# Kernel tuning notes

Hardware: AMD Instinct MI355X
Metric: run time of the kernel (lower is better)

Reference implementation:

```python
import jax, jax.numpy as jnp
import numpy as np

THR_CONF = 0.5   # threshold_conf
THR_NMS = 0.3    # threshold_nms
K = 1024         # fixed pre-NMS top-k per image (jit-friendly stand-in for boolean filter)
VAR0, VAR1 = 0.1, 0.2  # SSD/RetinaFace decode variances


def setup_inputs() -> dict:
    key = jax.random.key(0)
    k1, k2, k3, k4 = jax.random.split(key, 4)
    B, N = 64, 16800
    p_loc = jax.random.normal(k1, (B, N, 4), jnp.float32)
    p_conf = jax.random.normal(k2, (B, N, 1), jnp.float32)
    p_landms = jax.random.normal(k3, (B, N, 10), jnp.float32)
    # anchor priors in cxcywh, normalized coords
    anchors = jax.random.uniform(k4, (N, 4), jnp.float32, 0.05, 0.6)
    return {"p_loc": p_loc, "p_conf": p_conf, "p_landms": p_landms, "anchors": anchors}


def _decode_boxes(anchors, loc):
    # fix_bbox: cxcy = a_cxcy + loc_xy * var0 * a_wh ; wh = a_wh * exp(loc_wh * var1)
    xy = anchors[..., :2] + loc[..., :2] * VAR0 * anchors[..., 2:]
    wh = anchors[..., 2:] * jnp.exp(loc[..., 2:] * VAR1)
    # xywh2ltrb
    return jnp.concatenate([xy - wh * 0.5, xy + wh * 0.5], axis=-1)  # (B,N,4)


def _decode_kpts(anchors, landms):
    # fix_keypoints: 5 points, each = a_cxcy + d * var0 * a_wh
    B, N, _ = landms.shape
    pts = landms.reshape(B, N, 5, 2)
    kp = anchors[:, None, :2] + pts * VAR0 * anchors[:, None, 2:]
    return kp.reshape(B, N, 10)


def _iou_matrix(b):  # b: (K,4) ltrb -> (K,K)
    area = jnp.maximum(b[:, 2] - b[:, 0], 0.0) * jnp.maximum(b[:, 3] - b[:, 1], 0.0)
    lt = jnp.maximum(b[:, None, :2], b[None, :, :2])
    rb = jnp.minimum(b[:, None, 2:], b[None, :, 2:])
    wh = jnp.maximum(rb - lt, 0.0)
    inter = wh[..., 0] * wh[..., 1]
    return inter / (area[:, None] + area[None, :] - inter + 1e-9)


def _nms_one(boxes, kpts, scores):
    # boxes (N,4), kpts (N,10), scores (N,)
    s = jnp.where(scores >= THR_CONF, scores, -1.0)  # conf mask
    vals, idx = jax.lax.top_k(s, K)                  # sorted candidates (torch nms sorts by score)
    b = boxes[idx]
    kp = kpts[idx]
    iou = _iou_matrix(b)
    ar = jnp.arange(K)

    def body(suppressed, i):
        keep_i = (vals[i] >= THR_CONF) & (~suppressed[i])
        suppressed = suppressed | (keep_i & (iou[i] > THR_NMS) & (ar > i))
        return suppressed, keep_i

    _, keep = jax.lax.scan(body, jnp.zeros(K, dtype=bool), ar)
    m = keep.astype(b.dtype)[:, None]
    # (K,15) = ltrb(4) | keypoints(10) | score(1), zeroed where suppressed/filtered
    return jnp.concatenate([b, kp, vals[:, None]], axis=-1) * m


def reference(p_loc, p_conf, p_landms, anchors):
    scores = jax.nn.sigmoid(p_conf)[..., 0]       # (B,N)
    boxes = _decode_boxes(anchors, p_loc)         # (B,N,4) ltrb
    kpts = _decode_kpts(anchors, p_landms)        # (B,N,10)
    return jax.vmap(_nms_one)(boxes, kpts, scores)  # (B,K,15)
```

## Files before the change

kernel.cpp:

```cpp
#include <hip/hip_runtime.h>
#include <cmath>

#define NB 64
#define NN 16800
#define KK 1024
#define NT 1024
#define CAP 2048
#define RQ 17

typedef unsigned long long ull;

__device__ __forceinline__ unsigned int score_key_f(float cf) {
  if (!(cf >= 0.0f)) return 0u;
  return (__float_as_uint(cf) & 0x7FFFFFFFu) + 1u;
}

__device__ __forceinline__ unsigned int bin_of_key(unsigned int key) {
  float cf = __uint_as_float(key - 1u);
  unsigned int bi = (unsigned int)(int)(cf * 1024.0f);
  return bi > 4095u ? 4095u : bi;
}

__device__ __forceinline__ ull score_key_d(float cf) {
  double s = 1.0 / (1.0 + exp(-(double)cf));
  if (!(s >= 0.5)) return 0ull;
  return ((ull)__double_as_longlong(s) & 0xFFFFFFFFFFFFFull) + 1ull;
}

__device__ __forceinline__ void decode_box_d(const float* lp, const float* ap,
                                             double& X0, double& Y0,
                                             double& X1, double& Y1,
                                             double& AR) {
#pragma clang fp contract(off)
  double l0 = (double)lp[0], l1 = (double)lp[1];
  double l2 = (double)lp[2], l3 = (double)lp[3];
  double a0 = (double)ap[0], a1 = (double)ap[1];
  double a2 = (double)ap[2], a3 = (double)ap[3];
  double xy0 = a0 + (l0 * 0.1) * a2;
  double xy1 = a1 + (l1 * 0.1) * a3;
  double w = a2 * exp(l2 * 0.2);
  double h = a3 * exp(l3 * 0.2);
  X0 = xy0 - w * 0.5; Y0 = xy1 - h * 0.5;
  X1 = xy0 + w * 0.5; Y1 = xy1 + h * 0.5;
  AR = fmax(X1 - X0, 0.0) * fmax(Y1 - Y0, 0.0);
}

__device__ __forceinline__ bool iou_gt_d(double i0, double i1, double i2,
                                         double i3, double ia, double j0,
                                         double j1, double j2, double j3,
                                         double ja) {
#pragma clang fp contract(off)
  double lt0 = fmax(i0, j0), lt1 = fmax(i1, j1);
  double rb0 = fmin(i2, j2), rb1 = fmin(i3, j3);
  double w0 = fmax(rb0 - lt0, 0.0), w1 = fmax(rb1 - lt1, 0.0);
  double inter = w0 * w1;
  double den = ((ia + ja) - inter) + 1e-9;
  return (inter / den) > 0.3;
}

__global__ __launch_bounds__(1024, 1) void sort_kernel(
    const float* __restrict__ p_loc, const float* __restrict__ p_conf,
    const float* __restrict__ anchors, unsigned int* __restrict__ sidx_s,
    float* __restrict__ fbox, float* __restrict__ sval) {
  const int b = blockIdx.x;
  const int tid = threadIdx.x;
  const int lane = tid & 63;
  const int wave = tid >> 6;

  __shared__ unsigned int skey[CAP];
  __shared__ unsigned int sidx[CAP];
  __shared__ unsigned int hist[4096];
  __shared__ unsigned int base[4096];
  __shared__ unsigned int totals[64], chcarry[64];
  __shared__ unsigned int sh_found, sh_binT, sh_cB;
  __shared__ unsigned int scnt, sh_digit, sh_r, sh_c;

  const float* conf = p_conf + (size_t)b * NN;

  unsigned int rkey[RQ];
  #pragma unroll
  for (int q = 0; q < RQ; ++q) {
    const int i = tid + q * NT;
    rkey[q] = (i < NN) ? score_key_f(conf[i]) : 0u;
  }

  for (int i = tid; i < 4096; i += NT) hist[i] = 0u;
  if (tid == 0) sh_found = 0u;
  __syncthreads();
  #pragma unroll
  for (int q = 0; q < RQ; ++q) {
    unsigned int k = rkey[q];
    if (k != 0u) atomicAdd(&hist[bin_of_key(k)], 1u);
  }
  __syncthreads();
  for (int chunk = wave; chunk < 64; chunk += 16) {
    const int bin = chunk * 64 + (63 - lane);
    unsigned int c0 = hist[bin];
    unsigned int x = c0;
    #pragma unroll
    for (int d = 1; d < 64; d <<= 1) {
      unsigned int y = __shfl_up(x, d);
      if (lane >= d) x += y;
    }
    base[bin] = x;
    if (lane == 63) totals[chunk] = x;
  }
  __syncthreads();
  if (wave == 0) {
    const int chunk = 63 - lane;
    unsigned int t0 = totals[chunk];
    unsigned int x = t0;
    #pragma unroll
    for (int d = 1; d < 64; d <<= 1) {
      unsigned int y = __shfl_up(x, d);
      if (lane >= d) x += y;
    }
    chcarry[chunk] = x - t0;
  }
  __syncthreads();
  for (int chunk = wave; chunk < 64; chunk += 16) {
    const int bin = chunk * 64 + (63 - lane);
    unsigned int c0 = hist[bin];
    unsigned int S = chcarry[chunk] + base[bin] - c0;
    base[bin] = S;
    if (S < (unsigned)KK && (unsigned)KK <= S + c0) {
      sh_found = 1u; sh_binT = (unsigned int)bin; sh_cB = c0;
    }
  }
  __syncthreads();
  const bool fastOK = (sh_found != 0u) && (sh_cB <= 64u);
  const unsigned int binT = sh_binT;

  if (fastOK) {
    for (int i = tid; i < KK + 64; i += NT) { skey[i] = 0u; sidx[i] = 0xFFFFFFFFu; }
    __syncthreads();
    #pragma unroll
    for (int q = 0; q < RQ; ++q) {
      const int i = tid + q * NT;
      unsigned int k = rkey[q];
      if (k != 0u) {
        unsigned int bin = bin_of_key(k);
        if (bin >= binT) {
          unsigned int pos = atomicAdd(&base[bin], 1u);
          if (pos < (unsigned)(KK + 64)) { skey[pos] = k; sidx[pos] = (unsigned int)i; }
        }
      }
    }
    __syncthreads();
    for (int bin = (int)binT + tid; bin < 4096; bin += NT) {
      unsigned int cnt = hist[bin];
      if (cnt >= 2u) {
        int hi2 = (int)base[bin];
        int lo2 = hi2 - (int)cnt;
        for (int m2 = lo2 + 1; m2 < hi2; ++m2) {
          unsigned int kx = skey[m2]; unsigned int ix = sidx[m2];
          int n2 = m2;
          while (n2 > lo2) {
            unsigned int kp = skey[n2 - 1]; unsigned int ip = sidx[n2 - 1];
            bool after = (kp < kx) || (kp == kx && ip > ix);
            if (!after) break;
            skey[n2] = kp; sidx[n2] = ip; --n2;
          }
          skey[n2] = kx; sidx[n2] = ix;
        }
      }
    }
    __syncthreads();
  } else {
    unsigned int r = KK;
    unsigned int prefix = 0u, T = 0u;
    for (int pass = 0; pass < 4; ++pass) {
      const int shift = 24 - pass * 8;
      if (tid < 256) hist[tid] = 0u;
      __syncthreads();
      const unsigned int pm = pass ? ~((1u << (shift + 8)) - 1u) : 0u;
      #pragma unroll
      for (int q = 0; q < RQ; ++q) {
        unsigned int k = rkey[q];
        if (k != 0u && (k & pm) == prefix)
          atomicAdd(&hist[(k >> shift) & 255u], 1u);
      }
      __syncthreads();
      if (wave == 0) {
        if (lane == 0) { sh_digit = 0u; sh_r = r; sh_c = 0u; }
        unsigned int carry = 0;
        for (int chunk = 3; chunk >= 0; --chunk) {
          const int bin = chunk * 64 + (63 - lane);
          unsigned int c = hist[bin];
          unsigned int x = c;
          #pragma unroll
          for (int d = 1; d < 64; d <<= 1) {
            unsigned int y = __shfl_up(x, d);
            if (lane >= d) x += y;
          }
          unsigned int excl = x - c;
          unsigned int S = carry + excl;
          bool hit = (S < r) && (r <= S + c);
          ull bal = __ballot(hit ? 1 : 0);
          if (bal != 0ull) {
            int hl = __ffsll((long long)bal) - 1;
            unsigned int Sf = __shfl(S, hl);
            unsigned int bf = __shfl((unsigned int)bin, hl);
            unsigned int cf2 = __shfl(c, hl);
            if (lane == 0) { sh_digit = bf; sh_r = r - Sf; sh_c = cf2; }
            break;
          }
          carry += __shfl(x, 63);
        }
      }
      __syncthreads();
      prefix |= (sh_digit << shift);
      r = sh_r;
      const unsigned int cntge = (KK - r) + sh_c;
      if (cntge <= CAP || pass == 3) { T = prefix; break; }
    }

    if (tid == 0) scnt = 0u;
    for (int i = tid; i < CAP; i += NT) { skey[i] = 0u; sidx[i] = 0xFFFFFFFFu; }
    __syncthreads();
    #pragma unroll
    for (int q = 0; q < RQ; ++q) {
      const int i = tid + q * NT;
      unsigned int k = rkey[q];
      if (k != 0u && k >= T) {
        unsigned int pos = atomicAdd(&scnt, 1u);
        if (pos < CAP) { skey[pos] = k; sidx[pos] = (unsigned int)i; }
      }
    }
    __syncthreads();

    for (unsigned int k2 = 2; k2 <= CAP; k2 <<= 1) {
      for (unsigned int j = k2 >> 1; j > 0; j >>= 1) {
        for (int i = tid; i < CAP; i += NT) {
          int ixj = i ^ (int)j;
          if (ixj > i) {
            bool up = ((i & k2) == 0);
            unsigned int ka = skey[i], kbv = skey[ixj];
            unsigned int ia = sidx[i], ib = sidx[ixj];
            bool a_after_b = (ka < kbv) || (ka == kbv && ia > ib);
            if (a_after_b == up) {
              skey[i] = kbv; skey[ixj] = ka;
              sidx[i] = ib; sidx[ixj] = ia;
            }
          }
        }
        __syncthreads();
      }
    }
  }

  const unsigned int mykey = skey[tid];
  const unsigned int myidx = sidx[tid];
  double X0 = 0.0, Y0 = 0.0, X1 = 0.0, Y1 = 0.0, AR = 0.0;
  float v = -1.0f;
  if (mykey != 0u) {
    decode_box_d(p_loc + ((size_t)b * NN + myidx) * 4,
                 anchors + (size_t)myidx * 4, X0, Y0, X1, Y1, AR);
    double s = 1.0 / (1.0 + exp(-(double)conf[myidx]));
    v = (float)s;
  }
  sidx_s[(size_t)b * KK + tid] = myidx;
  float* fb = fbox + (size_t)b * 5 * KK;
  fb[0 * KK + tid] = (float)X0; fb[1 * KK + tid] = (float)Y0;
  fb[2 * KK + tid] = (float)X1; fb[3 * KK + tid] = (float)Y1;
  fb[4 * KK + tid] = (float)AR;
  sval[(size_t)b * KK + tid] = v;
}

__global__ __launch_bounds__(1024, 1) void nms_kernel(
    const float* __restrict__ p_loc, const float* __restrict__ p_landms,
    const float* __restrict__ anchors, const unsigned int* __restrict__ sidx_s,
    const float* __restrict__ fbox, const float* __restrict__ sval,
    float* __restrict__ out) {
  const int img = blockIdx.x, tid = threadIdx.x, lane = tid & 63,
            wave = tid >> 6;
  __shared__ float fb0[KK], fb1[KK], fb2[KK], fb3[KK], farr[KK];
  __shared__ float svbuf[KK];
  __shared__ unsigned int sxbuf[KK];
  __shared__ ull sup[16], mword[16], keepw[16], vmw[16];

  const float* fb = fbox + (size_t)img * 5 * KK;
  fb0[tid] = fb[0 * KK + tid]; fb1[tid] = fb[1 * KK + tid];
  fb2[tid] = fb[2 * KK + tid]; fb3[tid] = fb[3 * KK + tid];
  farr[tid] = fb[4 * KK + tid];
  svbuf[tid] = sval[(size_t)img * KK + tid];
  sxbuf[tid] = sidx_s[(size_t)img * KK + tid];
  if (tid < 16) { sup[tid] = 0ull; keepw[tid] = 0ull; }
  __syncthreads();
  {
    const ull vm = __ballot(svbuf[wave * 64 + lane] >= 0.0f);
    if (lane == 0) vmw[wave] = vm;
  }
  const float cj0 = fb0[tid], cj1 = fb1[tid], cj2 = fb2[tid], cj3 = fb3[tid];
  const float caj = farr[tid];
  const unsigned int cidx = sxbuf[tid];
  __syncthreads();

  for (int g = 0; g < 16; ++g) {
    ull supg = sup[g];
    const ull vmg = vmw[g];
    ull keepg = 0ull;
    for (int r = 0; r < 64; ++r) {
      const ull bm = 1ull << r;
      const bool keep = ((vmg & ~supg) & bm) != 0ull;
      if (keep) {
        const int i = g * 64 + r;
        keepg |= bm;
        const float bi0 = fb0[i], bi1 = fb1[i];
        const float bi2 = fb2[i], bi3 = fb3[i];
        const float ai = farr[i];
        float lt0 = fmaxf(bi0, cj0), lt1 = fmaxf(bi1, cj1);
        float q0 = fminf(bi2, cj2), q1 = fminf(bi3, cj3);
        float w0 = fmaxf(q0 - lt0, 0.0f), w1 = fmaxf(q1 - lt1, 0.0f);
        float inter = w0 * w1;
        float den = ((ai + caj) - inter) + 1e-9f;
        float d = inter - 0.3f * den;
        bool bit = d > 0.0f;
        bool unc = fabsf(d) <= den * 1e-3f;
        if (__builtin_expect((bool)__ballot(unc ? 1 : 0), 0)) {
          if (unc) {
            const unsigned int ridx = sxbuf[i];
            double rX0, rY0, rX1, rY1, rAR, qX0, qY0, qX1, qY1, qAR;
            decode_box_d(p_loc + ((size_t)img * NN + ridx) * 4,
                         anchors + (size_t)ridx * 4, rX0, rY0, rX1, rY1, rAR);
            decode_box_d(p_loc + ((size_t)img * NN + cidx) * 4,
                         anchors + (size_t)cidx * 4, qX0, qY0, qX1, qY1, qAR);
            bit = iou_gt_d(rX0, rY0, rX1, rY1, rAR, qX0, qY0, qX1, qY1, qAR);
          }
        }
        bit = bit && (tid > i);
        const ull m = __ballot(bit ? 1 : 0);
        if (lane == 0) mword[wave] = m;
        __syncthreads();
        supg |= mword[g];
        if (tid < 16) sup[tid] |= mword[tid];
        __syncthreads();
      }
    }
    if (tid == 0) keepw[g] = keepg;
  }
  __syncthreads();

  const bool keep = ((keepw[tid >> 6] >> (tid & 63)) & 1ull) != 0ull;
  float* op = out + ((size_t)img * KK + tid) * 15;
  if (keep) {
    op[0] = fb0[tid]; op[1] = fb1[tid];
    op[2] = fb2[tid]; op[3] = fb3[tid];
    const unsigned int myidx = sxbuf[tid];
    const float* pp = p_landms + ((size_t)img * NN + myidx) * 10;
    const float* ap = anchors + (size_t)myidx * 4;
    double a0 = (double)ap[0], a1 = (double)ap[1];
    double a2 = (double)ap[2], a3 = (double)ap[3];
    #pragma unroll
    for (int q = 0; q < 5; ++q) {
      double px = (double)pp[2 * q], py = (double)pp[2 * q + 1];
      op[4 + 2 * q]     = (float)(a0 + (px * 0.1) * a2);
      op[4 + 2 * q + 1] = (float)(a1 + (py * 0.1) * a3);
    }
    op[14] = svbuf[tid];
  } else {
    #pragma unroll
    for (int q = 0; q < 15; ++q) op[q] = 0.0f;
  }
}

__global__ __launch_bounds__(1024, 1) void fallback_kernel(
    const float* __restrict__ p_loc, const float* __restrict__ p_conf,
    const float* __restrict__ p_landms, const float* __restrict__ anchors,
    const ull* __restrict__ gkeys, float* __restrict__ out) {
  const int b = blockIdx.x;
  const int tid = threadIdx.x;
  const int lane = tid & 63;
  const int wave = tid >> 6;

  __shared__ ull skey[CAP];
  __shared__ unsigned int sidx[CAP];
  __shared__ float fb0[KK], fb1[KK], fb2[KK], fb3[KK], farr[KK];
  __shared__ float svalf[KK];
  __shared__ ull chunkmask[32][16];
  __shared__ unsigned int keepm[32];
  __shared__ ull supShared[16];
  __shared__ unsigned int hist[256];
  __shared__ unsigned int scnt, sh_digit, sh_r;

  unsigned long long rkey[RQ];
  if (gkeys != nullptr) {
    const ull* kb = gkeys + (size_t)b * NN;
    #pragma unroll
    for (int q = 0; q < RQ; ++q) {
      const int i = tid + q * NT;
      rkey[q] = (i < NN) ? kb[i] : 0ull;
    }
  } else {
    const float* conf = p_conf + (size_t)b * NN;
    #pragma unroll
    for (int q = 0; q < RQ; ++q) {
      const int i = tid + q * NT;
      rkey[q] = (i < NN) ? score_key_d(conf[i]) : 0ull;
    }
  }

  unsigned int r = KK;
  ull prefix = 0ull;
  for (int pass = 0; pass < 7; ++pass) {
    const int shift = 48 - pass * 8;
    if (tid < 256) hist[tid] = 0u;
    __syncthreads();
    const ull pm = (pass == 0) ? 0ull : ~((1ull << (shift + 8)) - 1ull);
    #pragma unroll
    for (int q = 0; q < RQ; ++q) {
      const int i = tid + q * NT;
      if (i < NN) {
        ull k = rkey[q];
        if (k != 0ull && (k & pm) == prefix)
          atomicAdd(&hist[(unsigned int)(k >> shift) & 255u], 1u);
      }
    }
    __syncthreads();
    if (wave == 0) {
      if (lane == 0) { sh_digit = 0u; sh_r = r; }
      unsigned int carry = 0;
      for (int chunk = 3; chunk >= 0; --chunk) {
        const int bin = chunk * 64 + (63 - lane);
        unsigned int c = hist[bin];
        unsigned int x = c;
        #pragma unroll
        for (int d = 1; d < 64; d <<= 1) {
          unsigned int y = __shfl_up(x, d);
          if (lane >= d) x += y;
        }
        unsigned int excl = x - c;
        unsigned int S = carry + excl;
        bool hit = (S < r) && (r <= S + c);
        ull bal = __ballot(hit ? 1 : 0);
        if (bal != 0ull) {
          int hl = __ffsll((long long)bal) - 1;
          unsigned int Sf = __shfl(S, hl);
          unsigned int bf = __shfl((unsigned int)bin, hl);
          if (lane == 0) { sh_digit = bf; sh_r = r - Sf; }
          break;
        }
        carry += __shfl(x, 63);
      }
    }
    __syncthreads();
    prefix |= ((ull)sh_digit << shift);
    r = sh_r;
    __syncthreads();
  }
  const ull T = prefix;

  if (tid == 0) scnt = 0u;
  for (int i = tid; i < CAP; i += NT) { skey[i] = 0ull; sidx[i] = 0xFFFFFFFFu; }
  __syncthreads();
  #pragma unroll
  for (int q = 0; q < RQ; ++q) {
    const int i = tid + q * NT;
    if (i < NN) {
      ull k = rkey[q];
      if (k != 0ull && k >= T) {
        unsigned int pos = atomicAdd(&scnt, 1u);
        if (pos < CAP) { skey[pos] = k; sidx[pos] = (unsigned int)i; }
      }
    }
  }
  __syncthreads();

  for (unsigned int k2 = 2; k2 <= CAP; k2 <<= 1) {
    for (unsigned int j = k2 >> 1; j > 0; j >>= 1) {
      for (int i = tid; i < CAP; i += NT) {
        int ixj = i ^ (int)j;
        if (ixj > i) {
          bool up = ((i & k2) == 0);
          ull ka = skey[i], kb = skey[ixj];
          unsigned int ia = sidx[i], ib = sidx[ixj];
          bool a_after_b = (ka < kb) || (ka == kb && ia > ib);
          if (a_after_b == up) {
            skey[i] = kb; skey[ixj] = ka;
            sidx[i] = ib; sidx[ixj] = ia;
          }
        }
      }
      __syncthreads();
    }
  }

  const ull mykey = skey[tid];
  const unsigned int myidx = sidx[tid];
  double dX0 = 0.0, dY0 = 0.0, dX1 = 0.0, dY1 = 0.0, dAR = 0.0;
  {
    float v = -1.0f;
    if (mykey != 0ull) {
      decode_box_d(p_loc + ((size_t)b * NN + myidx) * 4,
                   anchors + (size_t)myidx * 4, dX0, dY0, dX1, dY1, dAR);
      double s = __longlong_as_double(
          (long long)(0x3FE0000000000000ull | (mykey - 1ull)));
      v = (float)s;
    }
    fb0[tid] = (float)dX0; fb1[tid] = (float)dY0;
    fb2[tid] = (float)dX1; fb3[tid] = (float)dY1;
    farr[tid] = (float)dAR;
    svalf[tid] = v;
  }
  if (tid < 16) supShared[tid] = 0ull;
  if (tid < 32) keepm[tid] = 0u;
  __syncthreads();

  const float cj0 = fb0[tid], cj1 = fb1[tid], cj2 = fb2[tid], cj3 = fb3[tid];
  const float caj = farr[tid];
  ull supw = 0ull;

  for (int c = 0; c < 32; ++c) {
    for (int rr = 0; rr < 32; ++rr) {
      const int i = c * 32 + rr;
      const bool rowDead =
          (svalf[i] < 0.0f) ||
          (((supShared[i >> 6] >> (i & 63)) & 1ull) != 0ull);
      if (rowDead) continue;
      float bi0 = fb0[i], bi1 = fb1[i], bi2 = fb2[i], bi3 = fb3[i];
      float ai = farr[i];
      float lt0 = fmaxf(bi0, cj0), lt1 = fmaxf(bi1, cj1);
      float q0 = fminf(bi2, cj2), q1 = fminf(bi3, cj3);
      float w0 = fmaxf(q0 - lt0, 0.0f), w1 = fmaxf(q1 - lt1, 0.0f);
      float inter = w0 * w1;
      float den = ((ai + caj) - inter) + 1e-9f;
      float d = inter - 0.3f * den;
      bool bit = d > 0.0f;
      bool unc = fabsf(d) <= den * 1e-3f;
      if (__builtin_expect((bool)__ballot(unc ? 1 : 0), 0)) {
        if (unc) {
          const unsigned int ridx = sidx[i];
          double rX0, rY0, rX1, rY1, rAR;
          decode_box_d(p_loc + ((size_t)b * NN + ridx) * 4,
                       anchors + (size_t)ridx * 4, rX0, rY0, rX1, rY1, rAR);
          bit = iou_gt_d(rX0, rY0, rX1, rY1, rAR, dX0, dY0, dX1, dY1, dAR);
        }
      }
      bit = bit && (tid > i);
      ull m = __ballot(bit ? 1 : 0);
      if (lane == 0) chunkmask[rr][wave] = m;
    }
    __syncthreads();
    if (wave == 0) {
      unsigned int km = 0u;
      for (int rr = 0; rr < 32; ++rr) {
        const int i = c * 32 + rr;
        ull sc = __shfl(supw, i >> 6);
        bool keep = (svalf[i] >= 0.0f) && (((sc >> (i & 63)) & 1ull) == 0ull);
        if (keep) {
          km |= (1u << rr);
          if (lane < 16) supw |= chunkmask[rr][lane];
        }
      }
      if (lane == 0) keepm[c] = km;
      if (lane < 16) supShared[lane] = supw;
    }
    __syncthreads();
  }

  {
    const bool keep = ((keepm[tid >> 5] >> (tid & 31)) & 1u) != 0u;
    float* op = out + ((size_t)b * KK + tid) * 15;
    if (keep) {
      op[0] = fb0[tid]; op[1] = fb1[tid]; op[2] = fb2[tid]; op[3] = fb3[tid];
      const float* pp = p_landms + ((size_t)b * NN + myidx) * 10;
      const float* ap = anchors + (size_t)myidx * 4;
      double a0 = (double)ap[0], a1 = (double)ap[1];
      double a2 = (double)ap[2], a3 = (double)ap[3];
      #pragma unroll
      for (int q = 0; q < 5; ++q) {
        double px = (double)pp[2 * q], py = (double)pp[2 * q + 1];
        op[4 + 2 * q]     = (float)(a0 + (px * 0.1) * a2);
        op[4 + 2 * q + 1] = (float)(a1 + (py * 0.1) * a3);
      }
      op[14] = svalf[tid];
    } else {
      #pragma unroll
      for (int q = 0; q < 15; ++q) op[q] = 0.0f;
    }
  }
}

extern "C" void kernel_launch(void* const* d_in, const int* in_sizes, int n_in,
                              void* d_out, int out_size, void* d_ws, size_t ws_size,
                              hipStream_t stream) {
  const float* p_loc    = (const float*)d_in[0];
  const float* p_conf   = (const float*)d_in[1];
  const float* p_landms = (const float*)d_in[2];
  const float* anchors  = (const float*)d_in[3];
  float* out = (float*)d_out;
  (void)in_sizes; (void)n_in; (void)out_size;

  const size_t off_sidx = 0;
  const size_t off_fbox = off_sidx + (size_t)NB * KK * 4;
  const size_t off_sval = off_fbox + (size_t)NB * 5 * KK * 4;
  const size_t total = off_sval + (size_t)NB * KK * 4;

  char* ws = (char*)d_ws;

  if (ws_size >= total) {
    unsigned int* sidx_s = (unsigned int*)(ws + off_sidx);
    float* fbox = (float*)(ws + off_fbox);
    float* sval = (float*)(ws + off_sval);

    hipLaunchKernelGGL(sort_kernel, dim3(NB), dim3(NT), 0, stream,
                       p_loc, p_conf, anchors, sidx_s, fbox, sval);
    hipLaunchKernelGGL(nms_kernel, dim3(NB), dim3(NT), 0, stream,
                       p_loc, p_landms, anchors, sidx_s, fbox, sval, out);
  } else {
    hipLaunchKernelGGL(fallback_kernel, dim3(NB), dim3(NT), 0, stream,
                       p_loc, p_conf, p_landms, anchors, (const ull*)nullptr,
                       out);
  }
}
```

Baseline: 223.6 us.

## Fuse sort and NMS kernels into one per-image kernel with aliased LDS

Merges the sort kernel's front end with the fallback kernel's NMS and output stage into a single kernel per image. The decoded boxes, areas and scores now stay in shared memory instead of going through a global workspace, which removes one launch and the global write and read between stages. Histogram buffers share LDS with the box arrays and chunk masks, and the NMS switches to the fallback's chunked-mask scheme. The risk is higher shared-memory use per block and a different NMS loop structure, which could be slower than the old ballot-based one.

New measurement: 309.6 us. 38.5% more time.

```diff
diff --git a/kernel.cpp b/kernel.cpp
--- a/kernel.cpp
+++ b/kernel.cpp
@@ -19,12 +19,6 @@
   float cf = __uint_as_float(key - 1u);
   unsigned int bi = (unsigned int)(int)(cf * 1024.0f);
   return bi > 4095u ? 4095u : bi;
-}
-
-__device__ __forceinline__ ull score_key_d(float cf) {
-  double s = 1.0 / (1.0 + exp(-(double)cf));
-  if (!(s >= 0.5)) return 0ull;
-  return ((ull)__double_as_longlong(s) & 0xFFFFFFFFFFFFFull) + 1ull;
 }
 
 __device__ __forceinline__ void decode_box_d(const float* lp, const float* ap,
@@ -58,10 +52,10 @@
   return (inter / den) > 0.3;
 }
 
-__global__ __launch_bounds__(1024, 1) void sort_kernel(
+__global__ __launch_bounds__(1024, 1) void mono_kernel(
     const float* __restrict__ p_loc, const float* __restrict__ p_conf,
-    const float* __restrict__ anchors, unsigned int* __restrict__ sidx_s,
-    float* __restrict__ fbox, float* __restrict__ sval) {
+    const float* __restrict__ p_landms, const float* __restrict__ anchors,
+    float* __restrict__ out) {
   const int b = blockIdx.x;
   const int tid = threadIdx.x;
   const int lane = tid & 63;
@@ -69,11 +63,22 @@
 
   __shared__ unsigned int skey[CAP];
   __shared__ unsigned int sidx[CAP];
-  __shared__ unsigned int hist[4096];
-  __shared__ unsigned int base[4096];
+  __shared__ char uni[32768];
+  __shared__ float svalf[KK];
   __shared__ unsigned int totals[64], chcarry[64];
+  __shared__ unsigned int keepm[32];
+  __shared__ ull supShared[16];
   __shared__ unsigned int sh_found, sh_binT, sh_cB;
   __shared__ unsigned int scnt, sh_digit, sh_r, sh_c;
+
+  unsigned int* hist = reinterpret_cast<unsigned int*>(uni);
+  unsigned int* base = reinterpret_cast<unsigned int*>(uni + 16384);
+  float* fb0 = reinterpret_cast<float*>(uni);
+  float* fb1 = reinterpret_cast<float*>(uni + 4096);
+  float* fb2 = reinterpret_cast<float*>(uni + 8192);
+  float* fb3 = reinterpret_cast<float*>(uni + 12288);
+  float* farr = reinterpret_cast<float*>(uni + 16384);
+  ull (*chunkmask)[16] = reinterpret_cast<ull (*)[16]>(uni + 20480);
 
   const float* conf = p_conf + (size_t)b * NN;
 
@@ -251,250 +256,13 @@
 
   const unsigned int mykey = skey[tid];
   const unsigned int myidx = sidx[tid];
-  double X0 = 0.0, Y0 = 0.0, X1 = 0.0, Y1 = 0.0, AR = 0.0;
-  float v = -1.0f;
-  if (mykey != 0u) {
-    decode_box_d(p_loc + ((size_t)b * NN + myidx) * 4,
-                 anchors + (size_t)myidx * 4, X0, Y0, X1, Y1, AR);
-    double s = 1.0 / (1.0 + exp(-(double)conf[myidx]));
-    v = (float)s;
-  }
-  sidx_s[(size_t)b * KK + tid] = myidx;
-  float* fb = fbox + (size_t)b * 5 * KK;
-  fb[0 * KK + tid] = (float)X0; fb[1 * KK + tid] = (float)Y0;
-  fb[2 * KK + tid] = (float)X1; fb[3 * KK + tid] = (float)Y1;
-  fb[4 * KK + tid] = (float)AR;
-  sval[(size_t)b * KK + tid] = v;
-}
-
-__global__ __launch_bounds__(1024, 1) void nms_kernel(
-    const float* __restrict__ p_loc, const float* __restrict__ p_landms,
-    const float* __restrict__ anchors, const unsigned int* __restrict__ sidx_s,
-    const float* __restrict__ fbox, const float* __restrict__ sval,
-    float* __restrict__ out) {
-  const int img = blockIdx.x, tid = threadIdx.x, lane = tid & 63,
-            wave = tid >> 6;
-  __shared__ float fb0[KK], fb1[KK], fb2[KK], fb3[KK], farr[KK];
-  __shared__ float svbuf[KK];
-  __shared__ unsigned int sxbuf[KK];
-  __shared__ ull sup[16], mword[16], keepw[16], vmw[16];
-
-  const float* fb = fbox + (size_t)img * 5 * KK;
-  fb0[tid] = fb[0 * KK + tid]; fb1[tid] = fb[1 * KK + tid];
-  fb2[tid] = fb[2 * KK + tid]; fb3[tid] = fb[3 * KK + tid];
-  farr[tid] = fb[4 * KK + tid];
-  svbuf[tid] = sval[(size_t)img * KK + tid];
-  sxbuf[tid] = sidx_s[(size_t)img * KK + tid];
-  if (tid < 16) { sup[tid] = 0ull; keepw[tid] = 0ull; }
-  __syncthreads();
-  {
-    const ull vm = __ballot(svbuf[wave * 64 + lane] >= 0.0f);
-    if (lane == 0) vmw[wave] = vm;
-  }
-  const float cj0 = fb0[tid], cj1 = fb1[tid], cj2 = fb2[tid], cj3 = fb3[tid];
-  const float caj = farr[tid];
-  const unsigned int cidx = sxbuf[tid];
-  __syncthreads();
-
-  for (int g = 0; g < 16; ++g) {
-    ull supg = sup[g];
-    const ull vmg = vmw[g];
-    ull keepg = 0ull;
-    for (int r = 0; r < 64; ++r) {
-      const ull bm = 1ull << r;
-      const bool keep = ((vmg & ~supg) & bm) != 0ull;
-      if (keep) {
-        const int i = g * 64 + r;
-        keepg |= bm;
-        const float bi0 = fb0[i], bi1 = fb1[i];
-        const float bi2 = fb2[i], bi3 = fb3[i];
-        const float ai = farr[i];
-        float lt0 = fmaxf(bi0, cj0), lt1 = fmaxf(bi1, cj1);
-        float q0 = fminf(bi2, cj2), q1 = fminf(bi3, cj3);
-        float w0 = fmaxf(q0 - lt0, 0.0f), w1 = fmaxf(q1 - lt1, 0.0f);
-        float inter = w0 * w1;
-        float den = ((ai + caj) - inter) + 1e-9f;
-        float d = inter - 0.3f * den;
-        bool bit = d > 0.0f;
-        bool unc = fabsf(d) <= den * 1e-3f;
-        if (__builtin_expect((bool)__ballot(unc ? 1 : 0), 0)) {
-          if (unc) {
-            const unsigned int ridx = sxbuf[i];
-            double rX0, rY0, rX1, rY1, rAR, qX0, qY0, qX1, qY1, qAR;
-            decode_box_d(p_loc + ((size_t)img * NN + ridx) * 4,
-                         anchors + (size_t)ridx * 4, rX0, rY0, rX1, rY1, rAR);
-            decode_box_d(p_loc + ((size_t)img * NN + cidx) * 4,
-                         anchors + (size_t)cidx * 4, qX0, qY0, qX1, qY1, qAR);
-            bit = iou_gt_d(rX0, rY0, rX1, rY1, rAR, qX0, qY0, qX1, qY1, qAR);
-          }
-        }
-        bit = bit && (tid > i);
-        const ull m = __ballot(bit ? 1 : 0);
-        if (lane == 0) mword[wave] = m;
-        __syncthreads();
-        supg |= mword[g];
-        if (tid < 16) sup[tid] |= mword[tid];
-        __syncthreads();
-      }
-    }
-    if (tid == 0) keepw[g] = keepg;
-  }
-  __syncthreads();
-
-  const bool keep = ((keepw[tid >> 6] >> (tid & 63)) & 1ull) != 0ull;
-  float* op = out + ((size_t)img * KK + tid) * 15;
-  if (keep) {
-    op[0] = fb0[tid]; op[1] = fb1[tid];
-    op[2] = fb2[tid]; op[3] = fb3[tid];
-    const unsigned int myidx = sxbuf[tid];
-    const float* pp = p_landms + ((size_t)img * NN + myidx) * 10;
-    const float* ap = anchors + (size_t)myidx * 4;
-    double a0 = (double)ap[0], a1 = (double)ap[1];
-    double a2 = (double)ap[2], a3 = (double)ap[3];
-    #pragma unroll
-    for (int q = 0; q < 5; ++q) {
-      double px = (double)pp[2 * q], py = (double)pp[2 * q + 1];
-      op[4 + 2 * q]     = (float)(a0 + (px * 0.1) * a2);
-      op[4 + 2 * q + 1] = (float)(a1 + (py * 0.1) * a3);
-    }
-    op[14] = svbuf[tid];
-  } else {
-    #pragma unroll
-    for (int q = 0; q < 15; ++q) op[q] = 0.0f;
-  }
-}
-
-__global__ __launch_bounds__(1024, 1) void fallback_kernel(
-    const float* __restrict__ p_loc, const float* __restrict__ p_conf,
-    const float* __restrict__ p_landms, const float* __restrict__ anchors,
-    const ull* __restrict__ gkeys, float* __restrict__ out) {
-  const int b = blockIdx.x;
-  const int tid = threadIdx.x;
-  const int lane = tid & 63;
-  const int wave = tid >> 6;
-
-  __shared__ ull skey[CAP];
-  __shared__ unsigned int sidx[CAP];
-  __shared__ float fb0[KK], fb1[KK], fb2[KK], fb3[KK], farr[KK];
-  __shared__ float svalf[KK];
-  __shared__ ull chunkmask[32][16];
-  __shared__ unsigned int keepm[32];
-  __shared__ ull supShared[16];
-  __shared__ unsigned int hist[256];
-  __shared__ unsigned int scnt, sh_digit, sh_r;
-
-  unsigned long long rkey[RQ];
-  if (gkeys != nullptr) {
-    const ull* kb = gkeys + (size_t)b * NN;
-    #pragma unroll
-    for (int q = 0; q < RQ; ++q) {
-      const int i = tid + q * NT;
-      rkey[q] = (i < NN) ? kb[i] : 0ull;
-    }
-  } else {
-    const float* conf = p_conf + (size_t)b * NN;
-    #pragma unroll
-    for (int q = 0; q < RQ; ++q) {
-      const int i = tid + q * NT;
-      rkey[q] = (i < NN) ? score_key_d(conf[i]) : 0ull;
-    }
-  }
-
-  unsigned int r = KK;
-  ull prefix = 0ull;
-  for (int pass = 0; pass < 7; ++pass) {
-    const int shift = 48 - pass * 8;
-    if (tid < 256) hist[tid] = 0u;
-    __syncthreads();
-    const ull pm = (pass == 0) ? 0ull : ~((1ull << (shift + 8)) - 1ull);
-    #pragma unroll
-    for (int q = 0; q < RQ; ++q) {
-      const int i = tid + q * NT;
-      if (i < NN) {
-        ull k = rkey[q];
-        if (k != 0ull && (k & pm) == prefix)
-          atomicAdd(&hist[(unsigned int)(k >> shift) & 255u], 1u);
-      }
-    }
-    __syncthreads();
-    if (wave == 0) {
-      if (lane == 0) { sh_digit = 0u; sh_r = r; }
-      unsigned int carry = 0;
-      for (int chunk = 3; chunk >= 0; --chunk) {
-        const int bin = chunk * 64 + (63 - lane);
-        unsigned int c = hist[bin];
-        unsigned int x = c;
-        #pragma unroll
-        for (int d = 1; d < 64; d <<= 1) {
-          unsigned int y = __shfl_up(x, d);
-          if (lane >= d) x += y;
-        }
-        unsigned int excl = x - c;
-        unsigned int S = carry + excl;
-        bool hit = (S < r) && (r <= S + c);
-        ull bal = __ballot(hit ? 1 : 0);
-        if (bal != 0ull) {
-          int hl = __ffsll((long long)bal) - 1;
-          unsigned int Sf = __shfl(S, hl);
-          unsigned int bf = __shfl((unsigned int)bin, hl);
-          if (lane == 0) { sh_digit = bf; sh_r = r - Sf; }
-          break;
-        }
-        carry += __shfl(x, 63);
-      }
-    }
-    __syncthreads();
-    prefix |= ((ull)sh_digit << shift);
-    r = sh_r;
-    __syncthreads();
-  }
-  const ull T = prefix;
-
-  if (tid == 0) scnt = 0u;
-  for (int i = tid; i < CAP; i += NT) { skey[i] = 0ull; sidx[i] = 0xFFFFFFFFu; }
-  __syncthreads();
-  #pragma unroll
-  for (int q = 0; q < RQ; ++q) {
-    const int i = tid + q * NT;
-    if (i < NN) {
-      ull k = rkey[q];
-      if (k != 0ull && k >= T) {
-        unsigned int pos = atomicAdd(&scnt, 1u);
-        if (pos < CAP) { skey[pos] = k; sidx[pos] = (unsigned int)i; }
-      }
-    }
-  }
-  __syncthreads();
-
-  for (unsigned int k2 = 2; k2 <= CAP; k2 <<= 1) {
-    for (unsigned int j = k2 >> 1; j > 0; j >>= 1) {
-      for (int i = tid; i < CAP; i += NT) {
-        int ixj = i ^ (int)j;
-        if (ixj > i) {
-          bool up = ((i & k2) == 0);
-          ull ka = skey[i], kb = skey[ixj];
-          unsigned int ia = sidx[i], ib = sidx[ixj];
-          bool a_after_b = (ka < kb) || (ka == kb && ia > ib);
-          if (a_after_b == up) {
-            skey[i] = kb; skey[ixj] = ka;
-            sidx[i] = ib; sidx[ixj] = ia;
-          }
-        }
-      }
-      __syncthreads();
-    }
-  }
-
-  const ull mykey = skey[tid];
-  const unsigned int myidx = sidx[tid];
   double dX0 = 0.0, dY0 = 0.0, dX1 = 0.0, dY1 = 0.0, dAR = 0.0;
   {
     float v = -1.0f;
-    if (mykey != 0ull) {
+    if (mykey != 0u) {
       decode_box_d(p_loc + ((size_t)b * NN + myidx) * 4,
                    anchors + (size_t)myidx * 4, dX0, dY0, dX1, dY1, dAR);
-      double s = __longlong_as_double(
-          (long long)(0x3FE0000000000000ull | (mykey - 1ull)));
+      double s = 1.0 / (1.0 + exp(-(double)conf[myidx]));
       v = (float)s;
     }
     fb0[tid] = (float)dX0; fb1[tid] = (float)dY0;
@@ -589,27 +357,8 @@
   const float* p_landms = (const float*)d_in[2];
   const float* anchors  = (const float*)d_in[3];
   float* out = (float*)d_out;
-  (void)in_sizes; (void)n_in; (void)out_size;
-
-  const size_t off_sidx = 0;
-  const size_t off_fbox = off_sidx + (size_t)NB * KK * 4;
-  const size_t off_sval = off_fbox + (size_t)NB * 5 * KK * 4;
-  const size_t total = off_sval + (size_t)NB * KK * 4;
-
-  char* ws = (char*)d_ws;
-
-  if (ws_size >= total) {
-    unsigned int* sidx_s = (unsigned int*)(ws + off_sidx);
-    float* fbox = (float*)(ws + off_fbox);
-    float* sval = (float*)(ws + off_sval);
-
-    hipLaunchKernelGGL(sort_kernel, dim3(NB), dim3(NT), 0, stream,
-                       p_loc, p_conf, anchors, sidx_s, fbox, sval);
-    hipLaunchKernelGGL(nms_kernel, dim3(NB), dim3(NT), 0, stream,
-                       p_loc, p_landms, anchors, sidx_s, fbox, sval, out);
-  } else {
-    hipLaunchKernelGGL(fallback_kernel, dim3(NB), dim3(NT), 0, stream,
-                       p_loc, p_conf, p_landms, anchors, (const ull*)nullptr,
-                       out);
-  }
-}
+  (void)in_sizes; (void)n_in; (void)out_size; (void)d_ws; (void)ws_size;
+
+  hipLaunchKernelGGL(mono_kernel, dim3(NB), dim3(NT), 0, stream,
+                     p_loc, p_conf, p_landms, anchors, out);
+}
```
